# Optimization experiments

Hardware: AMD Instinct MI355X
Metric: run time of the kernel (lower is better)

The kernel has to match this reference:

```python
import jax, jax.numpy as jnp
import numpy as np


def setup_inputs() -> dict:
    key = jax.random.key(0)
    k1, k2 = jax.random.split(key)
    N, K, D = 262144, 1024, 256
    z_e = jax.random.normal(k1, (N, D), dtype=jnp.float32)
    # torch init: uniform(-1/num_embeddings, 1/num_embeddings)
    codebook = jax.random.uniform(k2, (K, D), dtype=jnp.float32,
                                  minval=-1.0 / K, maxval=1.0 / K)
    return {"z_e": z_e, "codebook": codebook}


def reference(z_e, codebook):
    # distances: ||z||^2 + ||c||^2 - 2 z c^T  -> [N, K]
    distances = (jnp.sum(z_e ** 2, axis=1, keepdims=True)
                 + jnp.sum(codebook ** 2, axis=1)
                 - 2.0 * jnp.matmul(z_e, codebook.T))
    min_encoding_indices = jnp.argmin(distances, axis=1)[:, None]  # [N, 1]
    z_q = codebook[min_encoding_indices[:, 0]]  # [N, D]

    # loss_vq = mse(z_q.detach(), z_e)
    loss_vq = jnp.mean((jax.lax.stop_gradient(z_q) - z_e) ** 2)

    # loss_mean = mse(z_e, mean_codebook.detach())
    mean_codebook = jnp.mean(codebook, axis=0)  # [D]
    loss_mean = jnp.mean((z_e - jax.lax.stop_gradient(mean_codebook)) ** 2)

    # straight-through estimator
    z_q_st = z_e + jax.lax.stop_gradient(z_q - z_e)
    return (z_q_st, loss_vq, loss_mean, min_encoding_indices)
```

## Files before the change

kernel.cpp:

```cpp
#include <hip/hip_runtime.h>


#define NROWS 262144
#define KCODES 1024
#define DDIM 256
#define ND ((size_t)NROWS * (size_t)DDIM)
#define M1F 6e-4f

typedef unsigned int uint;
typedef _Float16 f16x8 __attribute__((ext_vector_type(8)));
typedef float f32x4v __attribute__((ext_vector_type(4)));

__device__ inline float fadd(float a, float b) {
    float d; asm("v_add_f32 %0, %1, %2" : "=v"(d) : "v"(a), "v"(b)); return d;
}
__device__ inline float fmul(float a, float b) {
    float d; asm("v_mul_f32 %0, %1, %2" : "=v"(d) : "v"(a), "v"(b)); return d;
}
__device__ inline float fsub(float a, float b) {
    float d; asm("v_sub_f32 %0, %1, %2" : "=v"(d) : "v"(a), "v"(b)); return d;
}
__device__ inline float ffma(float a, float b, float c) {
    float d; asm("v_fma_f32 %0, %1, %2, %3" : "=v"(d) : "v"(a), "v"(b), "v"(c)); return d;
}

__device__ float np_sq_sum256(const float* __restrict__ a) {
    float tot[2];
    #pragma unroll 1
    for (int h = 0; h < 2; ++h) {
        const float* p = a + h * 128;
        float r[8];
        #pragma unroll
        for (int j = 0; j < 8; ++j) r[j] = fmul(p[j], p[j]);
        #pragma unroll 1
        for (int i = 8; i < 128; i += 8)
            #pragma unroll
            for (int j = 0; j < 8; ++j) r[j] = fadd(r[j], fmul(p[i + j], p[i + j]));
        tot[h] = fadd(fadd(fadd(r[0], r[1]), fadd(r[2], r[3])),
                      fadd(fadd(r[4], r[5]), fadd(r[6], r[7])));
    }
    return fadd(tot[0], tot[1]);
}

__device__ float blas_dot256(const float* __restrict__ zr, const float* __restrict__ cr) {
    float dot = 0.f;
    #pragma unroll 4
    for (int d4 = 0; d4 < 64; ++d4) {
        float4 zz = *(const float4*)(zr + d4 * 4);
        float4 cc = *(const float4*)(cr + d4 * 4);
        dot = ffma(zz.x, cc.x, dot); dot = ffma(zz.y, cc.y, dot);
        dot = ffma(zz.z, cc.z, dot); dot = ffma(zz.w, cc.w, dot);
    }
    return dot;
}

__global__ void k_prep(const float* __restrict__ cb, char* __restrict__ cbh,
                       float* __restrict__ scp, float* __restrict__ mAcc) {
    int bx = blockIdx.x;
    if (bx < 128) {
        int g = bx * 256 + threadIdx.x;
        int t = g >> 11, c = (g >> 5) & 63, j = g & 31;
        const float* s = cb + (size_t)(t * 64 + c) * DDIM + j * 8;
        float4 v0 = *(const float4*)s, v1 = *(const float4*)(s + 4);
        f16x8 h;
        h[0] = (_Float16)(v0.x * 1024.f); h[1] = (_Float16)(v0.y * 1024.f);
        h[2] = (_Float16)(v0.z * 1024.f); h[3] = (_Float16)(v0.w * 1024.f);
        h[4] = (_Float16)(v1.x * 1024.f); h[5] = (_Float16)(v1.y * 1024.f);
        h[6] = (_Float16)(v1.z * 1024.f); h[7] = (_Float16)(v1.w * 1024.f);
        uint byte = (uint)(c * 512 + j * 16) ^ (uint)((c & 7) << 4);
        *(f16x8*)(cbh + (size_t)t * 32768 + byte) = h;
    } else if (bx < 132) {
        int code = (bx - 128) * 256 + threadIdx.x;
        if (code < KCODES) scp[code] = np_sq_sum256(cb + (size_t)code * DDIM);
    } else {
        int d = threadIdx.x;
        int b = bx - 132;
        float s = 0.f;
        for (int i = 0; i < 64; ++i) s += cb[(size_t)(b * 64 + i) * DDIM + d];
        atomicAdd(&mAcc[d], s);
    }
}

__global__ void k_meanfin(const float* __restrict__ mAcc,
                          float* __restrict__ mvec, double* __restrict__ M2p) {
    __shared__ double red[256];
    int d = threadIdx.x;
    float m = mAcc[d] * (1.0f / 1024.0f);
    mvec[d] = m;
    red[d] = (double)m * (double)m;
    __syncthreads();
    for (int off = 128; off; off >>= 1) {
        if (d < off) red[d] += red[d + off];
        __syncthreads();
    }
    if (d == 0) *M2p = red[0];
}

#define GLOAD_LDS16(g, l) \
    __builtin_amdgcn_global_load_lds( \
        (const __attribute__((address_space(1))) void*)(g), \
        (__attribute__((address_space(3))) void*)(l), 16, 0, 0)

__launch_bounds__(256, 2)
__global__ void k_main(const float* __restrict__ z, const char* __restrict__ cbh,
                       const float* __restrict__ sc, const float* __restrict__ mvec,
                       float* __restrict__ out, uint* __restrict__ counts,
                       uint2* __restrict__ listTri, uint* __restrict__ listFull,
                       int capTri, int capFull,
                       double* __restrict__ lossA, double* __restrict__ lossB) {
    __shared__ char tiles[2][32768] __attribute__((aligned(16)));
    __shared__ float sc_lds[1024];
    __shared__ float statA[128], statZM[128];
    __shared__ float lred[2];

    const int tid = threadIdx.x;
    const int wave = tid >> 6;
    const int lane = tid & 63;
    const int l15 = lane & 15;
    const int lg = lane >> 4;
    const int blockRow = blockIdx.x * 128;

    if (tid < 2) lred[tid] = 0.f;
    for (int i = tid; i < 1024; i += 256) sc_lds[i] = sc[i];

    f16x8 za[2][8];
    #pragma unroll
    for (int m = 0; m < 2; ++m) {
        const float* zr = z + (size_t)(blockRow + wave * 32 + m * 16 + l15) * DDIM;
        float a2 = 0.f, zm = 0.f;
        #pragma unroll
        for (int kk = 0; kk < 8; ++kk) {
            int d0 = kk * 32 + lg * 8;
            float4 v0 = *(const float4*)(zr + d0);
            float4 v1 = *(const float4*)(zr + d0 + 4);
            float4 w0 = *(const float4*)(mvec + d0);
            float4 w1 = *(const float4*)(mvec + d0 + 4);
            a2 += v0.x * v0.x + v0.y * v0.y + v0.z * v0.z + v0.w * v0.w;
            a2 += v1.x * v1.x + v1.y * v1.y + v1.z * v1.z + v1.w * v1.w;
            zm += v0.x * w0.x + v0.y * w0.y + v0.z * w0.z + v0.w * w0.w;
            zm += v1.x * w1.x + v1.y * w1.y + v1.z * w1.z + v1.w * w1.w;
            f16x8 h;
            h[0] = (_Float16)v0.x; h[1] = (_Float16)v0.y;
            h[2] = (_Float16)v0.z; h[3] = (_Float16)v0.w;
            h[4] = (_Float16)v1.x; h[5] = (_Float16)v1.y;
            h[6] = (_Float16)v1.z; h[7] = (_Float16)v1.w;
            za[m][kk] = h;
        }
        a2 += __shfl_xor(a2, 16); a2 += __shfl_xor(a2, 32);
        zm += __shfl_xor(zm, 16); zm += __shfl_xor(zm, 32);
        if (lg == 0) {
            statA[wave * 32 + m * 16 + l15] = a2;
            statZM[wave * 32 + m * 16 + l15] = zm;
        }
    }
    __syncthreads();

    float k1v[2][4], k2v[2][4], k3v[2][4];
    #pragma unroll
    for (int m = 0; m < 2; ++m)
        #pragma unroll
        for (int r = 0; r < 4; ++r) { k1v[m][r] = 3e38f; k2v[m][r] = 3e38f; k3v[m][r] = 3e38f; }

    const char* gsrc0 = cbh + (size_t)wave * 1024 + (size_t)lane * 16;
    #define STAGE(T, BUF) { \
        const char* g_ = gsrc0 + (size_t)(T) * 32768; \
        char* l_ = &tiles[BUF][wave * 1024]; \
        _Pragma("unroll") \
        for (int i_ = 0; i_ < 8; ++i_) GLOAD_LDS16(g_ + i_ * 4096, l_ + i_ * 4096); \
    }

    #define COMPUTE(T, BUF) { \
        f32x4v acc[2][4]; \
        _Pragma("unroll") \
        for (int m = 0; m < 2; ++m) \
            _Pragma("unroll") \
            for (int n = 0; n < 4; ++n) acc[m][n] = (f32x4v){0.f, 0.f, 0.f, 0.f}; \
        const char* tb = &tiles[BUF][0]; \
        _Pragma("unroll") \
        for (int kk = 0; kk < 8; ++kk) { \
            _Pragma("unroll") \
            for (int n = 0; n < 4; ++n) { \
                int lcode = n * 16 + l15; \
                uint byte = (uint)(lcode * 512 + kk * 64 + lg * 16) ^ (uint)((lcode & 7) << 4); \
                f16x8 b = *(const f16x8*)(tb + byte); \
                acc[0][n] = __builtin_amdgcn_mfma_f32_16x16x32_f16(za[0][kk], b, acc[0][n], 0, 0, 0); \
                acc[1][n] = __builtin_amdgcn_mfma_f32_16x16x32_f16(za[1][kk], b, acc[1][n], 0, 0, 0); \
            } \
        } \
        int tbase = (T) * 64; \
        _Pragma("unroll") \
        for (int n = 0; n < 4; ++n) { \
            int codev = tbase + n * 16 + l15; \
            float scv = sc_lds[codev]; \
            _Pragma("unroll") \
            for (int m = 0; m < 2; ++m) \
                _Pragma("unroll") \
                for (int r = 0; r < 4; ++r) { \
                    float s = fmaf(acc[m][n][r], -0.001953125f, scv); \
                    uint kb = (__float_as_uint(s) & 0xFFFFFC00u) | (uint)codev; \
                    float k = __uint_as_float(kb); \
                    float o1 = k1v[m][r], o2 = k2v[m][r]; \
                    k3v[m][r] = __builtin_amdgcn_fmed3f(o2, k3v[m][r], k); \
                    k2v[m][r] = __builtin_amdgcn_fmed3f(o1, o2, k); \
                    k1v[m][r] = fminf(o1, k); \
                } \
        } \
    }

    STAGE(0, 0);
    #pragma unroll 1
    for (int t = 0; t < 15; ++t) {
        STAGE(t + 1, (t + 1) & 1);
        asm volatile("s_waitcnt vmcnt(8)" ::: "memory");
        __builtin_amdgcn_s_barrier();
        __builtin_amdgcn_sched_barrier(0);
        COMPUTE(t, t & 1);
        __builtin_amdgcn_sched_barrier(0);
        __builtin_amdgcn_s_barrier();
    }
    asm volatile("s_waitcnt vmcnt(0)" ::: "memory");
    __builtin_amdgcn_s_barrier();
    __builtin_amdgcn_sched_barrier(0);
    COMPUTE(15, 1);

    float lA = 0.f, lB = 0.f;
    #pragma unroll
    for (int m = 0; m < 2; ++m)
        #pragma unroll
        for (int r = 0; r < 4; ++r) {
            float a1 = k1v[m][r], a2 = k2v[m][r], a3 = k3v[m][r];
            #pragma unroll
            for (int mk = 1; mk <= 8; mk <<= 1) {
                float b1 = __shfl_xor(a1, mk);
                float b2 = __shfl_xor(a2, mk);
                float b3 = __shfl_xor(a3, mk);
                float mx = fmaxf(a1, b1);
                float n3 = fminf(fminf(__builtin_amdgcn_fmed3f(a2, b2, mx), a3), b3);
                float n2 = fminf(fminf(mx, a2), b2);
                a1 = fminf(a1, b1); a2 = n2; a3 = n3;
            }
            if (l15 == 0) {
                int rowL = wave * 32 + m * 16 + lg * 4 + r;
                int row = blockRow + rowL;
                int i1 = (int)(__float_as_uint(a1) & 1023u);
                int i2 = (int)(__float_as_uint(a2) & 1023u);
                int i3 = (int)(__float_as_uint(a3) & 1023u);
                int flag = (a3 - a1 < M1F) ? 2 : ((a2 - a1 < M1F) ? 1 : 0);
                float slotval = (float)i1;
                if (flag == 2) {
                    uint p = atomicAdd(&counts[1], 1u);
                    if (p < (uint)capFull) listFull[p] = (uint)row;
                    else slotval = (float)(i1 | (1 << 20));
                } else if (flag == 1) {
                    uint p = atomicAdd(&counts[0], 1u);
                    if (p < (uint)capTri)
                        listTri[p] = make_uint2((uint)row, (uint)(i1 | (i2 << 10) | (i3 << 20)));
                    else slotval = (float)(i1 | (1 << 20));
                }
                out[ND + 2 + (size_t)row] = slotval;
                lA += statA[rowL] + a1;
                lB += statA[rowL] - 2.f * statZM[rowL];
            }
        }
    if (l15 == 0) { atomicAdd(&lred[0], lA); atomicAdd(&lred[1], lB); }
    __syncthreads();
    if (tid == 0) {
        atomicAdd(lossA, (double)lred[0]);
        atomicAdd(lossB, (double)lred[1]);
    }
}

__global__ void k_gather(const float* __restrict__ cb, float* __restrict__ out) {
    __shared__ int idx[128];
    const int tid = threadIdx.x;
    const int blockRow = blockIdx.x * 128;
    if (tid < 128) idx[tid] = ((int)out[ND + 2 + (size_t)(blockRow + tid)]) & 1023;
    __syncthreads();
    float4* out4 = (float4*)out;
    const float4* cb4 = (const float4*)cb;
    #pragma unroll 4
    for (int i = 0; i < 32; ++i) {
        int q = i * 256 + tid;
        int rowL = q >> 6, ch = q & 63;
        int code = idx[rowL];
        out4[(size_t)(blockRow + rowL) * 64 + ch] = cb4[(size_t)code * 64 + ch];
    }
}

__launch_bounds__(256)
__global__ void k_refine_tri(const float* __restrict__ z, const float* __restrict__ cb,
                             const float* __restrict__ scp,
                             const uint* __restrict__ counts,
                             const uint2* __restrict__ listTri, int capTri,
                             float* __restrict__ out) {
    __shared__ float B[4][4][256];
    const int wv = threadIdx.x >> 6;
    const int lane = threadIdx.x & 63;
    uint n = counts[0];
    if (n > (uint)capTri) n = (uint)capTri;
    uint nw = gridDim.x * 4;
    for (uint it = blockIdx.x * 4 + wv; it < n; it += nw) {
        uint2 e = listTri[it];
        int row = (int)e.x;
        int i1 = (int)(e.y & 1023), i2 = (int)((e.y >> 10) & 1023), i3 = (int)((e.y >> 20) & 1023);
        *(float4*)&B[wv][0][lane * 4] = *(const float4*)(z + (size_t)row * DDIM + lane * 4);
        *(float4*)&B[wv][1][lane * 4] = *(const float4*)(cb + (size_t)i1 * DDIM + lane * 4);
        *(float4*)&B[wv][2][lane * 4] = *(const float4*)(cb + (size_t)i2 * DDIM + lane * 4);
        *(float4*)&B[wv][3][lane * 4] = *(const float4*)(cb + (size_t)i3 * DDIM + lane * 4);
        asm volatile("s_waitcnt vmcnt(0) lgkmcnt(0)" ::: "memory");
        __builtin_amdgcn_sched_barrier(0);
        float A = np_sq_sum256(B[wv][0]);
        float dA = 0.f, dB = 0.f, dC = 0.f;
        #pragma unroll 4
        for (int d4 = 0; d4 < 64; ++d4) {
            float4 zz = *(const float4*)&B[wv][0][d4 * 4];
            float4 ca = *(const float4*)&B[wv][1][d4 * 4];
            float4 cc = *(const float4*)&B[wv][2][d4 * 4];
            float4 cd = *(const float4*)&B[wv][3][d4 * 4];
            dA = ffma(zz.x, ca.x, dA); dA = ffma(zz.y, ca.y, dA);
            dA = ffma(zz.z, ca.z, dA); dA = ffma(zz.w, ca.w, dA);
            dB = ffma(zz.x, cc.x, dB); dB = ffma(zz.y, cc.y, dB);
            dB = ffma(zz.z, cc.z, dB); dB = ffma(zz.w, cc.w, dB);
            dC = ffma(zz.x, cd.x, dC); dC = ffma(zz.y, cd.y, dC);
            dC = ffma(zz.z, cd.z, dC); dC = ffma(zz.w, cd.w, dC);
        }
        float d1 = fsub(fadd(A, scp[i1]), fmul(2.f, dA));
        float d2 = fsub(fadd(A, scp[i2]), fmul(2.f, dB));
        float d3 = fsub(fadd(A, scp[i3]), fmul(2.f, dC));
        int win = i1; float bd = d1;
        if (d2 < bd || (d2 == bd && i2 < win)) { bd = d2; win = i2; }
        if (d3 < bd || (d3 == bd && i3 < win)) { bd = d3; win = i3; }
        if (win != i1) {
            if (lane == 0) out[ND + 2 + (size_t)row] = (float)win;
            *(float4*)(out + (size_t)row * DDIM + lane * 4) =
                *(const float4*)(cb + (size_t)win * DDIM + lane * 4);
        }
    }
}

__launch_bounds__(256, 2)
__global__ void k_refine_full(const float* __restrict__ z, const float* __restrict__ cb,
                              const float* __restrict__ scp,
                              const uint* __restrict__ counts,
                              const uint* __restrict__ listFull, int capFull,
                              float* __restrict__ out) {
    __shared__ float zrow[256];
    __shared__ float avs[256];
    __shared__ int ais[256];
    __shared__ int winsh;

    uint n = counts[1];
    if (n > (uint)capFull) n = (uint)capFull;
    const int tid = threadIdx.x;

    for (uint j = blockIdx.x; j < n; j += gridDim.x) {
        int row = (int)listFull[j];
        __syncthreads();
        if (tid < 64)
            *(float4*)&zrow[tid * 4] = *(const float4*)(z + (size_t)row * DDIM + tid * 4);
        __syncthreads();

        float A = np_sq_sum256(zrow);

        float d0 = 0.f, d1 = 0.f, d2 = 0.f, d3 = 0.f;
        const float* c0 = cb + (size_t)(tid + 0) * DDIM;
        const float* c1 = cb + (size_t)(tid + 256) * DDIM;
        const float* c2 = cb + (size_t)(tid + 512) * DDIM;
        const float* c3 = cb + (size_t)(tid + 768) * DDIM;
        #pragma unroll 4
        for (int q = 0; q < 64; ++q) {
            float4 zz = *(const float4*)&zrow[q * 4];
            float4 a = *(const float4*)(c0 + q * 4);
            float4 b = *(const float4*)(c1 + q * 4);
            float4 c = *(const float4*)(c2 + q * 4);
            float4 d = *(const float4*)(c3 + q * 4);
            d0 = ffma(zz.x, a.x, d0); d0 = ffma(zz.y, a.y, d0);
            d0 = ffma(zz.z, a.z, d0); d0 = ffma(zz.w, a.w, d0);
            d1 = ffma(zz.x, b.x, d1); d1 = ffma(zz.y, b.y, d1);
            d1 = ffma(zz.z, b.z, d1); d1 = ffma(zz.w, b.w, d1);
            d2 = ffma(zz.x, c.x, d2); d2 = ffma(zz.y, c.y, d2);
            d2 = ffma(zz.z, c.z, d2); d2 = ffma(zz.w, c.w, d2);
            d3 = ffma(zz.x, d.x, d3); d3 = ffma(zz.y, d.y, d3);
            d3 = ffma(zz.z, d.z, d3); d3 = ffma(zz.w, d.w, d3);
        }
        float best = 1e30f; int bi = 0x7fffffff;
        float dd[4] = {d0, d1, d2, d3};
        #pragma unroll
        for (int kk = 0; kk < 4; ++kk) {
            int code = tid + kk * 256;
            float dist = fsub(fadd(A, scp[code]), fmul(2.f, dd[kk]));
            if (dist < best || (dist == best && code < bi)) { best = dist; bi = code; }
        }
        avs[tid] = best; ais[tid] = bi;
        __syncthreads();
        for (int off = 128; off; off >>= 1) {
            if (tid < off) {
                float o = avs[tid + off]; int oi = ais[tid + off];
                if (o < avs[tid] || (o == avs[tid] && oi < ais[tid])) {
                    avs[tid] = o; ais[tid] = oi;
                }
            }
            __syncthreads();
        }
        if (tid == 0) {
            winsh = ais[0];
            out[ND + 2 + (size_t)row] = (float)ais[0];
        }
        __syncthreads();
        int win = winsh;
        out[(size_t)row * DDIM + tid] = cb[(size_t)win * DDIM + tid];
    }
}

__global__ void k_sweep(const float* __restrict__ z, const float* __restrict__ cb,
                        const float* __restrict__ scp, float* __restrict__ out) {
    int row = blockIdx.x * 256 + threadIdx.x;
    float v = out[ND + 2 + (size_t)row];
    if (v < 1048576.f) return;
    int enc = (int)v;
    int i1 = enc & 1023;
    const float* zr = z + (size_t)row * DDIM;
    float A = np_sq_sum256(zr);
    float best = 1e30f; int win = 0x7fffffff;
    for (int code = 0; code < KCODES; ++code) {
        float dot = blas_dot256(zr, cb + (size_t)code * DDIM);
        float dist = fsub(fadd(A, scp[code]), fmul(2.f, dot));
        if (dist < best) { best = dist; win = code; }
    }
    out[ND + 2 + (size_t)row] = (float)win;
    if (win != i1) {
        const float4* cw = (const float4*)(cb + (size_t)win * DDIM);
        float4* ow = (float4*)(out + (size_t)row * DDIM);
        for (int c = 0; c < 64; ++c) ow[c] = cw[c];
    }
}

__global__ void k_final(const double* __restrict__ lossA, const double* __restrict__ lossB,
                        const double* __restrict__ M2p, float* __restrict__ out) {
    if (threadIdx.x == 0) {
        double nd = (double)ND;
        out[ND] = (float)(*lossA / nd);
        out[ND + 1] = (float)((*lossB + (double)NROWS * (*M2p)) / nd);
    }
}

extern "C" void kernel_launch(void* const* d_in, const int* in_sizes, int n_in,
                              void* d_out, int out_size, void* d_ws, size_t ws_size,
                              hipStream_t stream) {
    const float* z = (const float*)d_in[0];
    const float* cb = (const float*)d_in[1];
    float* out = (float*)d_out;

    double* lossA = (double*)d_ws;
    double* lossB = lossA + 1;
    double* M2p   = lossA + 2;
    uint*   counts = (uint*)((char*)d_ws + 24);
    float*  mAcc  = (float*)((char*)d_ws + 32);
    float*  mvec  = (float*)((char*)d_ws + 2048);
    float*  scp   = (float*)((char*)d_ws + 4096);
    char*   cbh   = (char*)d_ws + 8192;

    size_t base = 8192 + 524288;
    size_t avail = ws_size > base ? ws_size - base : 0;
    int capFull = (int)(avail / 24);
    if (capFull > 32768) capFull = 32768;
    size_t fullBytes = ((size_t)capFull * 4 + 7) & ~(size_t)7;
    size_t availTri = avail > fullBytes ? avail - fullBytes : 0;
    int capTri = (int)(availTri / 8);
    if (capTri > 131072) capTri = 131072;

    uint*  listFull = (uint*)((char*)d_ws + base);
    uint2* listTri  = (uint2*)((char*)d_ws + base + fullBytes);

    hipMemsetAsync(d_ws, 0, 1056, stream);
    k_prep<<<148, 256, 0, stream>>>(cb, cbh, scp, mAcc);
    k_meanfin<<<1, 256, 0, stream>>>(mAcc, mvec, M2p);
    k_main<<<NROWS / 128, 256, 0, stream>>>(z, cbh, scp, mvec, out,
                                            counts, listTri, listFull,
                                            capTri, capFull, lossA, lossB);
    k_gather<<<NROWS / 128, 256, 0, stream>>>(cb, out);
    k_refine_tri<<<512, 256, 0, stream>>>(z, cb, scp, counts, listTri, capTri, out);
    k_refine_full<<<1024, 256, 0, stream>>>(z, cb, scp, counts, listFull, capFull, out);
    k_sweep<<<NROWS / 256, 256, 0, stream>>>(z, cb, scp, out);
    k_final<<<1, 64, 0, stream>>>(lossA, lossB, M2p, out);
}
```

Before: 905.5 us.

## Halve codebook tile size to raise occupancy to four blocks per CU

The codebook staging tile shrinks from 64 to 32 codes (16KB per buffer), so the loop runs 32 iterations instead of 16, and the launch bound goes from 2 to 4 blocks per CU. The top-3 trackers are split per n-subtile and merged before the cross-lane reduction. s_setprio is raised around the MFMA section so waves doing matrix work get issue priority. This trades fewer MFMAs per barrier and a tighter register budget for more resident waves to hide load and barrier latency.

New measurement: 1.256 ms. 38.7% more time.

```diff
diff --git a/kernel.cpp b/kernel.cpp
--- a/kernel.cpp
+++ b/kernel.cpp
@@ -59,8 +59,8 @@
     int bx = blockIdx.x;
     if (bx < 128) {
         int g = bx * 256 + threadIdx.x;
-        int t = g >> 11, c = (g >> 5) & 63, j = g & 31;
-        const float* s = cb + (size_t)(t * 64 + c) * DDIM + j * 8;
+        int t = g >> 10, c = (g >> 5) & 31, j = g & 31;
+        const float* s = cb + (size_t)(t * 32 + c) * DDIM + j * 8;
         float4 v0 = *(const float4*)s, v1 = *(const float4*)(s + 4);
         f16x8 h;
         h[0] = (_Float16)(v0.x * 1024.f); h[1] = (_Float16)(v0.y * 1024.f);
@@ -68,7 +68,7 @@
         h[4] = (_Float16)(v1.x * 1024.f); h[5] = (_Float16)(v1.y * 1024.f);
         h[6] = (_Float16)(v1.z * 1024.f); h[7] = (_Float16)(v1.w * 1024.f);
         uint byte = (uint)(c * 512 + j * 16) ^ (uint)((c & 7) << 4);
-        *(f16x8*)(cbh + (size_t)t * 32768 + byte) = h;
+        *(f16x8*)(cbh + (size_t)t * 16384 + byte) = h;
     } else if (bx < 132) {
         int code = (bx - 128) * 256 + threadIdx.x;
         if (code < KCODES) scp[code] = np_sq_sum256(cb + (size_t)code * DDIM);
@@ -101,14 +101,14 @@
         (const __attribute__((address_space(1))) void*)(g), \
         (__attribute__((address_space(3))) void*)(l), 16, 0, 0)
 
-__launch_bounds__(256, 2)
+__launch_bounds__(256, 4)
 __global__ void k_main(const float* __restrict__ z, const char* __restrict__ cbh,
                        const float* __restrict__ sc, const float* __restrict__ mvec,
                        float* __restrict__ out, uint* __restrict__ counts,
                        uint2* __restrict__ listTri, uint* __restrict__ listFull,
                        int capTri, int capFull,
                        double* __restrict__ lossA, double* __restrict__ lossB) {
-    __shared__ char tiles[2][32768] __attribute__((aligned(16)));
+    __shared__ char tiles[2][16384] __attribute__((aligned(16)));
     __shared__ float sc_lds[1024];
     __shared__ float statA[128], statZM[128];
     __shared__ float lred[2];
@@ -155,31 +155,36 @@
     }
     __syncthreads();
 
-    float k1v[2][4], k2v[2][4], k3v[2][4];
+    float k1v[2][2][4], k2v[2][2][4], k3v[2][2][4];
     #pragma unroll
-    for (int m = 0; m < 2; ++m)
+    for (int n = 0; n < 2; ++n)
         #pragma unroll
-        for (int r = 0; r < 4; ++r) { k1v[m][r] = 3e38f; k2v[m][r] = 3e38f; k3v[m][r] = 3e38f; }
-
-    const char* gsrc0 = cbh + (size_t)wave * 1024 + (size_t)lane * 16;
+        for (int m = 0; m < 2; ++m)
+            #pragma unroll
+            for (int r = 0; r < 4; ++r) {
+                k1v[n][m][r] = 3e38f; k2v[n][m][r] = 3e38f; k3v[n][m][r] = 3e38f;
+            }
+
+    const char* gsrc0 = cbh + (size_t)wave * 4096 + (size_t)lane * 16;
     #define STAGE(T, BUF) { \
-        const char* g_ = gsrc0 + (size_t)(T) * 32768; \
-        char* l_ = &tiles[BUF][wave * 1024]; \
+        const char* g_ = gsrc0 + (size_t)(T) * 16384; \
+        char* l_ = &tiles[BUF][wave * 4096]; \
         _Pragma("unroll") \
-        for (int i_ = 0; i_ < 8; ++i_) GLOAD_LDS16(g_ + i_ * 4096, l_ + i_ * 4096); \
+        for (int i_ = 0; i_ < 4; ++i_) GLOAD_LDS16(g_ + i_ * 1024, l_ + i_ * 1024); \
     }
 
     #define COMPUTE(T, BUF) { \
-        f32x4v acc[2][4]; \
+        f32x4v acc[2][2]; \
         _Pragma("unroll") \
         for (int m = 0; m < 2; ++m) \
             _Pragma("unroll") \
-            for (int n = 0; n < 4; ++n) acc[m][n] = (f32x4v){0.f, 0.f, 0.f, 0.f}; \
+            for (int n = 0; n < 2; ++n) acc[m][n] = (f32x4v){0.f, 0.f, 0.f, 0.f}; \
         const char* tb = &tiles[BUF][0]; \
+        __builtin_amdgcn_s_setprio(1); \
         _Pragma("unroll") \
         for (int kk = 0; kk < 8; ++kk) { \
             _Pragma("unroll") \
-            for (int n = 0; n < 4; ++n) { \
+            for (int n = 0; n < 2; ++n) { \
                 int lcode = n * 16 + l15; \
                 uint byte = (uint)(lcode * 512 + kk * 64 + lg * 16) ^ (uint)((lcode & 7) << 4); \
                 f16x8 b = *(const f16x8*)(tb + byte); \
@@ -187,9 +192,10 @@
                 acc[1][n] = __builtin_amdgcn_mfma_f32_16x16x32_f16(za[1][kk], b, acc[1][n], 0, 0, 0); \
             } \
         } \
-        int tbase = (T) * 64; \
+        __builtin_amdgcn_s_setprio(0); \
+        int tbase = (T) * 32; \
         _Pragma("unroll") \
-        for (int n = 0; n < 4; ++n) { \
+        for (int n = 0; n < 2; ++n) { \
             int codev = tbase + n * 16 + l15; \
             float scv = sc_lds[codev]; \
             _Pragma("unroll") \
@@ -199,19 +205,19 @@
                     float s = fmaf(acc[m][n][r], -0.001953125f, scv); \
                     uint kb = (__float_as_uint(s) & 0xFFFFFC00u) | (uint)codev; \
                     float k = __uint_as_float(kb); \
-                    float o1 = k1v[m][r], o2 = k2v[m][r]; \
-                    k3v[m][r] = __builtin_amdgcn_fmed3f(o2, k3v[m][r], k); \
-                    k2v[m][r] = __builtin_amdgcn_fmed3f(o1, o2, k); \
-                    k1v[m][r] = fminf(o1, k); \
+                    float o1 = k1v[n][m][r], o2 = k2v[n][m][r]; \
+                    k3v[n][m][r] = __builtin_amdgcn_fmed3f(o2, k3v[n][m][r], k); \
+                    k2v[n][m][r] = __builtin_amdgcn_fmed3f(o1, o2, k); \
+                    k1v[n][m][r] = fminf(o1, k); \
                 } \
         } \
     }
 
     STAGE(0, 0);
     #pragma unroll 1
-    for (int t = 0; t < 15; ++t) {
+    for (int t = 0; t < 31; ++t) {
         STAGE(t + 1, (t + 1) & 1);
-        asm volatile("s_waitcnt vmcnt(8)" ::: "memory");
+        asm volatile("s_waitcnt vmcnt(4)" ::: "memory");
         __builtin_amdgcn_s_barrier();
         __builtin_amdgcn_sched_barrier(0);
         COMPUTE(t, t & 1);
@@ -221,22 +227,27 @@
     asm volatile("s_waitcnt vmcnt(0)" ::: "memory");
     __builtin_amdgcn_s_barrier();
     __builtin_amdgcn_sched_barrier(0);
-    COMPUTE(15, 1);
+    COMPUTE(31, 1);
 
     float lA = 0.f, lB = 0.f;
     #pragma unroll
     for (int m = 0; m < 2; ++m)
         #pragma unroll
         for (int r = 0; r < 4; ++r) {
-            float a1 = k1v[m][r], a2 = k2v[m][r], a3 = k3v[m][r];
+            float x1 = k1v[0][m][r], x2 = k2v[0][m][r], x3 = k3v[0][m][r];
+            float y1 = k1v[1][m][r], y2 = k2v[1][m][r], y3 = k3v[1][m][r];
+            float mx = fmaxf(x1, y1);
+            float a3 = fminf(fminf(__builtin_amdgcn_fmed3f(x2, y2, mx), x3), y3);
+            float a2 = fminf(fminf(mx, x2), y2);
+            float a1 = fminf(x1, y1);
             #pragma unroll
             for (int mk = 1; mk <= 8; mk <<= 1) {
                 float b1 = __shfl_xor(a1, mk);
                 float b2 = __shfl_xor(a2, mk);
                 float b3 = __shfl_xor(a3, mk);
-                float mx = fmaxf(a1, b1);
-                float n3 = fminf(fminf(__builtin_amdgcn_fmed3f(a2, b2, mx), a3), b3);
-                float n2 = fminf(fminf(mx, a2), b2);
+                float mx2 = fmaxf(a1, b1);
+                float n3 = fminf(fminf(__builtin_amdgcn_fmed3f(a2, b2, mx2), a3), b3);
+                float n2 = fminf(fminf(mx2, a2), b2);
                 a1 = fminf(a1, b1); a2 = n2; a3 = n3;
             }
             if (l15 == 0) {
```
